# Kernel tuning notes

Hardware: AMD Instinct MI355X
Metric: run time of the kernel (lower is better)

## Reference

```python
import jax, jax.numpy as jnp
import numpy as np

D = 1024      # model dim
NSEQ = 4      # packed sequences
SEQ = 8192    # tokens per sequence
L = NSEQ * SEQ
EPS = 1e-4    # prob clamp in dechunk


def setup_inputs() -> dict:
    key = jax.random.key(0)
    ks = jax.random.split(key, 7)
    s = 1.0 / np.sqrt(D)
    mk = lambda k: jax.random.normal(k, (D, D), jnp.float32) * s
    return {
        'x': jax.random.normal(ks[0], (1, L, D), jnp.float32),
        'Wq': mk(ks[1]), 'Wk': mk(ks[2]), 'Wr': mk(ks[3]),
        'We': mk(ks[4]), 'Wm': mk(ks[5]), 'Wd': mk(ks[6]),
        'cu_seqlens': jnp.arange(NSEQ + 1, dtype=jnp.int32) * SEQ,
    }


def _normalize(v):
    n = jnp.linalg.norm(v, axis=-1, keepdims=True)
    return v / jnp.maximum(n, 1e-12)


def _forward(x, Wq, Wk, Wr, We, Wm, Wd, cu_seqlens):
    # encoder (pointwise linear)
    enc = jnp.einsum('bld,ed->ble', x, We)                  # [1,L,D]
    residual = jnp.einsum('bld,ed->ble', enc, Wr)           # residual_proj

    # Router: cosine similarity of adjacent tokens
    q = _normalize(jnp.einsum('bld,ed->ble', enc[:, :-1], Wq))
    k = _normalize(jnp.einsum('bld,ed->ble', enc[:, 1:], Wk))
    p = 0.5 * (1.0 - jnp.sum(q * k, axis=-1))               # [1,L-1]
    p = jnp.pad(p, ((0, 0), (1, 0)), constant_values=1.0)[0]  # [L]
    p = p.at[cu_seqlens[:-1]].set(1.0)                      # force boundary at seq starts
    mask = p > 0.5                                          # boundary_mask
    sel = jnp.where(mask, p, 1.0 - p)                       # selected_prob

    # main network on compressed tokens (pointwise -> compute in full layout,
    # non-boundary positions are never read by the scan below)
    m = jnp.einsum('bld,ed->ble', enc, Wm)[0]               # [L,D]

    # dechunk == mamba scan with A=-1, N=1: EMA h_t=(1-p)h + p*u at boundaries,
    # held (a=1) elsewhere; plug_back gather == held state. Reset at seq starts.
    pc = jnp.clip(p, EPS, 1.0 - EPS)
    starts = jnp.zeros(L, bool).at[cu_seqlens[:-1]].set(True)
    a = jnp.where(starts, 0.0, jnp.where(mask, 1.0 - pc, 1.0))[:, None]  # [L,1]
    b = jnp.where(mask[:, None], pc[:, None] * m, 0.0)                    # [L,D]

    def comb(c1, c2):
        a1, b1 = c1
        a2, b2 = c2
        return (a1 * a2, a2 * b1 + b2)

    _, y = jax.lax.associative_scan(comb, (a, b), axis=0)   # y: [L,D] dechunked

    # straight-through: forward multiplies by 1, backward passes grad to sel
    st = sel + jax.lax.stop_gradient(1.0 - sel)
    out = y[None] * st[None, :, None] + residual
    out = jnp.einsum('bld,ed->ble', out, Wd)                # decoder
    return out


def reference(x, Wq, Wk, Wr, We, Wm, Wd, cu_seqlens):
    return _forward(x, Wq, Wk, Wr, We, Wm, Wd, cu_seqlens)
```

## Files before the change

kernel.cpp:

```cpp
#include <hip/hip_runtime.h>
#include <math.h>

#define D_DIM 1024
#define CL 512

typedef __attribute__((ext_vector_type(8))) short short8;
typedef __attribute__((ext_vector_type(4))) float f32x4;
typedef unsigned short u16;

__device__ __forceinline__ u16 f2bf(float f) {
    unsigned int u = __float_as_uint(f);
    u += 0x7fff + ((u >> 16) & 1);
    return (u16)(u >> 16);
}
__device__ __forceinline__ float bf2f(u16 h) {
    return __uint_as_float((unsigned int)h << 16);
}

#define GLOAD16(g, l) __builtin_amdgcn_global_load_lds(                      \
        (const __attribute__((address_space(1))) void*)(g),                  \
        (__attribute__((address_space(3))) void*)(l), 16, 0, 0)
#define SBAR()   __builtin_amdgcn_s_barrier()
#define SCHED0() __builtin_amdgcn_sched_barrier(0)
#define PRIO(x)  __builtin_amdgcn_s_setprio(x)
#define WAITVM(N) asm volatile("s_waitcnt vmcnt(" #N ")" ::: "memory")


template<int EPI, int NPAIR>
__global__ __launch_bounds__(512) void gemm256(const u16* __restrict__ A1,
                                               const u16* __restrict__ W1,
                                               const u16* __restrict__ A2,
                                               const u16* __restrict__ W2,
                                               float* __restrict__ Cf,
                                               u16* __restrict__ Cb) {
    constexpr int NT = NPAIR * 32;
    __shared__ u16 lds[4 * 16384];
    __shared__ float nsum[4][256];
    const int tid = threadIdx.x;
    const int lane = tid & 63, wid = tid >> 6;
    const int wm = wid >> 2, wn = wid & 3;
    const int fr = lane & 15, fq = lane >> 4;
    const int row0 = blockIdx.x * 256, col0 = blockIdx.y * 256;
    const int r0s = tid >> 2, c0s = tid & 3;

    int offA[8], offB[4];
#pragma unroll
    for (int i = 0; i < 8; ++i) {
        const int r = wm * 128 + i * 16 + fr;
        offA[i] = r * 64 + ((fq ^ ((r >> 1) & 3)) << 4);
    }
#pragma unroll
    for (int j = 0; j < 4; ++j) {
        const int r = wn * 64 + j * 16 + fr;
        offB[j] = r * 64 + ((fq ^ ((r >> 1) & 3)) << 4);
    }

    auto stageA = [&](int s) {
        const u16* src = (NPAIR == 2 && s >= 32) ? A2 : A1;
        const int k0 = (NPAIR == 2 ? (s & 31) : s) * 32;
        char* dst = (char*)lds + (s & 3) * 32768;
#pragma unroll
        for (int j = 0; j < 2; ++j) {
            const int r = j * 128 + r0s;
            const int c = c0s ^ ((r >> 1) & 3);
            GLOAD16(src + (size_t)(row0 + r) * D_DIM + k0 + c * 8,
                    dst + j * 8192 + tid * 16);
        }
    };
    auto stageB = [&](int s) {
        const u16* src = (NPAIR == 2 && s >= 32) ? W2 : W1;
        const int k0 = (NPAIR == 2 ? (s & 31) : s) * 32;
        char* dst = (char*)lds + (s & 3) * 32768 + 16384;
#pragma unroll
        for (int j = 0; j < 2; ++j) {
            const int r = j * 128 + r0s;
            const int c = c0s ^ ((r >> 1) & 3);
            GLOAD16(src + (size_t)(col0 + r) * D_DIM + k0 + c * 8,
                    dst + j * 8192 + tid * 16);
        }
    };

    f32x4 acc[8][4];
#pragma unroll
    for (int i = 0; i < 8; ++i)
#pragma unroll
        for (int j = 0; j < 4; ++j) acc[i][j] = (f32x4){0.f, 0.f, 0.f, 0.f};

    stageA(0); stageB(0); stageA(1); stageB(1); stageA(2); stageB(2);
    WAITVM(8); SBAR(); SCHED0();

    for (int t = 0; t < NT; ++t) {
        const char* buf  = (const char*)lds + (t & 3) * 32768;
        const char* bufB = buf + 16384;
        short8 af[8], bf[4];
#pragma unroll
        for (int i = 0; i < 4; ++i) af[i] = *(const short8*)(buf + offA[i]);
#pragma unroll
        for (int j = 0; j < 4; ++j) bf[j] = *(const short8*)(bufB + offB[j]);
        if (t + 3 < NT) stageA(t + 3);
        SBAR();
        PRIO(1);
#pragma unroll
        for (int i = 0; i < 4; ++i)
#pragma unroll
            for (int j = 0; j < 4; ++j)
                acc[i][j] = __builtin_amdgcn_mfma_f32_16x16x32_bf16(af[i], bf[j], acc[i][j], 0, 0, 0);
        PRIO(0);
#pragma unroll
        for (int i = 4; i < 8; ++i) af[i] = *(const short8*)(buf + offA[i]);
        if (t + 3 < NT) stageB(t + 3);
        SBAR();
        PRIO(1);
#pragma unroll
        for (int i = 4; i < 8; ++i)
#pragma unroll
            for (int j = 0; j < 4; ++j)
                acc[i][j] = __builtin_amdgcn_mfma_f32_16x16x32_bf16(af[i], bf[j], acc[i][j], 0, 0, 0);
        PRIO(0);
        if (t + 1 < NT) {
            if (t + 3 < NT)      { WAITVM(8); }
            else if (t + 2 < NT) { WAITVM(4); }
            else                 { WAITVM(0); }
            SBAR(); SCHED0();
        }
    }

    if (EPI == 2) {
#pragma unroll
        for (int i = 0; i < 8; ++i)
#pragma unroll
            for (int rr = 0; rr < 4; ++rr) {
                float s = acc[i][0][rr] * acc[i][0][rr] + acc[i][1][rr] * acc[i][1][rr]
                        + acc[i][2][rr] * acc[i][2][rr] + acc[i][3][rr] * acc[i][3][rr];
#pragma unroll
                for (int off = 1; off < 16; off <<= 1) s += __shfl_xor(s, off);
                if (fr == 0) nsum[wn][wm * 128 + i * 16 + fq * 4 + rr] = s;
            }
        __syncthreads();
        if (tid < 256)
            Cf[(size_t)blockIdx.y * (gridDim.x * 256) + row0 + tid] =
                nsum[0][tid] + nsum[1][tid] + nsum[2][tid] + nsum[3][tid];
    } else {
#pragma unroll
        for (int i = 0; i < 8; ++i)
#pragma unroll
            for (int j = 0; j < 4; ++j) {
                const int r0 = row0 + wm * 128 + i * 16 + fq * 4;
                const int c  = col0 + wn * 64 + j * 16 + fr;
#pragma unroll
                for (int rr = 0; rr < 4; ++rr) {
                    if (EPI == 0) Cb[(size_t)(r0 + rr) * D_DIM + c] = f2bf(acc[i][j][rr]);
                    else          Cf[(size_t)(r0 + rr) * D_DIM + c] = acc[i][j][rr];
                }
            }
    }
}

template<int EPI>
__global__ __launch_bounds__(512) void gemm_x3(const u16* __restrict__ Ah,
                                               const u16* __restrict__ Al,
                                               const u16* __restrict__ Wh,
                                               const u16* __restrict__ Wl,
                                               float* __restrict__ Cf,
                                               u16* __restrict__ Chi,
                                               u16* __restrict__ Clo) {
    constexpr int NT = 32;
    __shared__ u16 lds[3 * 24576];
    const int tid = threadIdx.x;
    const int lane = tid & 63, wid = tid >> 6;
    const int wm = wid >> 2, wn = wid & 3;
    const int fr = lane & 15, fq = lane >> 4;
    const int row0 = blockIdx.x * 128, col0 = blockIdx.y * 256;
    const int r0s = tid >> 2, c0s = tid & 3;

    int offA[4], offB[4];
#pragma unroll
    for (int i = 0; i < 4; ++i) {
        const int r = wm * 64 + i * 16 + fr;
        offA[i] = r * 64 + ((fq ^ ((r >> 1) & 3)) << 4);
    }
#pragma unroll
    for (int j = 0; j < 4; ++j) {
        const int r = wn * 64 + j * 16 + fr;
        offB[j] = r * 64 + ((fq ^ ((r >> 1) & 3)) << 4);
    }

    auto stageAhl = [&](int s) {
        char* base = (char*)lds + (s % 3) * 49152;
        const int r = r0s;
        const int c = c0s ^ ((r >> 1) & 3);
        const size_t g = (size_t)(row0 + r) * D_DIM + s * 32 + c * 8;
        GLOAD16(Ah + g, base + tid * 16);
        GLOAD16(Al + g, base + 8192 + tid * 16);
    };
    auto stageBh = [&](int s) {
        char* base = (char*)lds + (s % 3) * 49152 + 16384;
#pragma unroll
        for (int j = 0; j < 2; ++j) {
            const int r = j * 128 + r0s;
            const int c = c0s ^ ((r >> 1) & 3);
            GLOAD16(Wh + (size_t)(col0 + r) * D_DIM + s * 32 + c * 8,
                    base + j * 8192 + tid * 16);
        }
    };
    auto stageBl = [&](int s) {
        char* base = (char*)lds + (s % 3) * 49152 + 32768;
#pragma unroll
        for (int j = 0; j < 2; ++j) {
            const int r = j * 128 + r0s;
            const int c = c0s ^ ((r >> 1) & 3);
            GLOAD16(Wl + (size_t)(col0 + r) * D_DIM + s * 32 + c * 8,
                    base + j * 8192 + tid * 16);
        }
    };

    f32x4 acc[4][4];
#pragma unroll
    for (int i = 0; i < 4; ++i)
#pragma unroll
        for (int j = 0; j < 4; ++j) acc[i][j] = (f32x4){0.f, 0.f, 0.f, 0.f};

    stageAhl(0); stageBh(0); stageBl(0);
    stageAhl(1); stageBh(1); stageBl(1);
    WAITVM(6); SBAR(); SCHED0();

    for (int t = 0; t < NT; ++t) {
        const char* base = (const char*)lds + (t % 3) * 49152;
        short8 afh[4], afl[4], bfh[4], bfl[4];
#pragma unroll
        for (int i = 0; i < 4; ++i) afh[i] = *(const short8*)(base + offA[i]);
#pragma unroll
        for (int j = 0; j < 4; ++j) bfh[j] = *(const short8*)(base + 16384 + offB[j]);
        if (t + 2 < NT) stageBh(t + 2);
        SBAR();
        PRIO(1);
#pragma unroll
        for (int i = 0; i < 4; ++i)
#pragma unroll
            for (int j = 0; j < 4; ++j)
                acc[i][j] = __builtin_amdgcn_mfma_f32_16x16x32_bf16(afh[i], bfh[j], acc[i][j], 0, 0, 0);
        PRIO(0);
#pragma unroll
        for (int j = 0; j < 4; ++j) bfl[j] = *(const short8*)(base + 32768 + offB[j]);
        if (t + 2 < NT) stageBl(t + 2);
        SBAR();
        PRIO(1);
#pragma unroll
        for (int i = 0; i < 4; ++i)
#pragma unroll
            for (int j = 0; j < 4; ++j)
                acc[i][j] = __builtin_amdgcn_mfma_f32_16x16x32_bf16(afh[i], bfl[j], acc[i][j], 0, 0, 0);
        PRIO(0);
#pragma unroll
        for (int i = 0; i < 4; ++i) afl[i] = *(const short8*)(base + 8192 + offA[i]);
        if (t + 2 < NT) stageAhl(t + 2);
        SBAR();
        PRIO(1);
#pragma unroll
        for (int i = 0; i < 4; ++i)
#pragma unroll
            for (int j = 0; j < 4; ++j)
                acc[i][j] = __builtin_amdgcn_mfma_f32_16x16x32_bf16(afl[i], bfh[j], acc[i][j], 0, 0, 0);
        PRIO(0);
        if (t + 1 < NT) {
            if (t + 2 < NT) { WAITVM(6); }
            else            { WAITVM(0); }
            SBAR(); SCHED0();
        }
    }

#pragma unroll
    for (int i = 0; i < 4; ++i)
#pragma unroll
        for (int j = 0; j < 4; ++j) {
            const int r0 = row0 + wm * 64 + i * 16 + fq * 4;
            const int c  = col0 + wn * 64 + j * 16 + fr;
#pragma unroll
            for (int rr = 0; rr < 4; ++rr) {
                const float v = acc[i][j][rr];
                if (EPI == 0) {
                    const u16 h = f2bf(v);
                    Chi[(size_t)(r0 + rr) * D_DIM + c] = h;
                    Clo[(size_t)(r0 + rr) * D_DIM + c] = f2bf(v - bf2f(h));
                } else {
                    Cf[(size_t)(r0 + rr) * D_DIM + c] = v;
                }
            }
        }
}

__global__ __launch_bounds__(256) void gemm_bf16_nt(const u16* __restrict__ A,
                                                    const u16* __restrict__ W,
                                                    float* __restrict__ C,
                                                    u16* __restrict__ Cbf) {
    __shared__ u16 lA[128 * 32];
    __shared__ u16 lB[128 * 32];
    const int tid  = threadIdx.x;
    const int lane = tid & 63, wid = tid >> 6;
    const int wy = wid & 1, wx = wid >> 1;
    const int fr = lane & 15, fq = lane >> 4;
    const int row0 = blockIdx.x * 128;
    const int col0 = blockIdx.y * 128;

    const int rS   = tid >> 2;
    const int subS = (tid & 3) ^ ((rS >> 1) & 3);
    const u16* gA = A + (size_t)(row0 + rS) * D_DIM + subS * 8;
    const u16* gB = W + (size_t)(col0 + rS) * D_DIM + subS * 8;
    char* lA0 = (char*)lA + tid * 16;
    char* lB0 = (char*)lB + tid * 16;
    const size_t rowStep = (size_t)64 * D_DIM;

    int offA[4], offB[4];
#pragma unroll
    for (int i = 0; i < 4; ++i) {
        const int ra = wy * 64 + i * 16 + fr;
        const int rb = wx * 64 + i * 16 + fr;
        offA[i] = ra * 64 + ((fq ^ ((ra >> 1) & 3)) << 4);
        offB[i] = rb * 64 + ((fq ^ ((rb >> 1) & 3)) << 4);
    }

    f32x4 acc[4][4];
#pragma unroll
    for (int i = 0; i < 4; ++i)
#pragma unroll
        for (int j = 0; j < 4; ++j) acc[i][j] = (f32x4){0.f, 0.f, 0.f, 0.f};

    for (int k0 = 0; k0 < D_DIM; k0 += 32) {
        __syncthreads();
        GLOAD16(gA + k0, lA0);
        GLOAD16(gA + k0 + rowStep, lA0 + 4096);
        GLOAD16(gB + k0, lB0);
        GLOAD16(gB + k0 + rowStep, lB0 + 4096);
        __syncthreads();
        short8 af[4], bf[4];
#pragma unroll
        for (int i = 0; i < 4; ++i) af[i] = *(const short8*)((const char*)lA + offA[i]);
#pragma unroll
        for (int j = 0; j < 4; ++j) bf[j] = *(const short8*)((const char*)lB + offB[j]);
#pragma unroll
        for (int i = 0; i < 4; ++i)
#pragma unroll
            for (int j = 0; j < 4; ++j)
                acc[i][j] = __builtin_amdgcn_mfma_f32_16x16x32_bf16(af[i], bf[j], acc[i][j], 0, 0, 0);
    }
#pragma unroll
    for (int i = 0; i < 4; ++i)
#pragma unroll
        for (int j = 0; j < 4; ++j) {
            const int r0 = row0 + wy * 64 + i * 16 + fq * 4;
            const int c  = col0 + wx * 64 + j * 16 + fr;
            if (Cbf) {
#pragma unroll
                for (int r = 0; r < 4; ++r)
                    Cbf[(size_t)(r0 + r) * D_DIM + c] = f2bf(acc[i][j][r]);
            } else {
#pragma unroll
                for (int r = 0; r < 4; ++r)
                    C[(size_t)(r0 + r) * D_DIM + c] = acc[i][j][r];
            }
        }
}

__global__ void split_bf16(const float* __restrict__ src, u16* __restrict__ hi,
                           u16* __restrict__ lo, int n4) {
    int i = blockIdx.x * 256 + threadIdx.x;
    if (i >= n4) return;
    float4 v = ((const float4*)src)[i];
    ushort4 h, l;
    h.x = f2bf(v.x); l.x = f2bf(v.x - bf2f(h.x));
    h.y = f2bf(v.y); l.y = f2bf(v.y - bf2f(h.y));
    h.z = f2bf(v.z); l.z = f2bf(v.z - bf2f(h.z));
    h.w = f2bf(v.w); l.w = f2bf(v.w - bf2f(h.w));
    ((ushort4*)hi)[i] = h;
    ((ushort4*)lo)[i] = l;
}

__global__ void conv_bf16(const float* __restrict__ src, u16* __restrict__ dst, int n4) {
    int i = blockIdx.x * 256 + threadIdx.x;
    if (i >= n4) return;
    float4 v = ((const float4*)src)[i];
    ushort4 o = {f2bf(v.x), f2bf(v.y), f2bf(v.z), f2bf(v.w)};
    ((ushort4*)dst)[i] = o;
}

__global__ __launch_bounds__(256) void transpose_split(const float* __restrict__ W,
                                                       u16* __restrict__ Th,
                                                       u16* __restrict__ Tl) {
    __shared__ float tile[32][33];
    const int e0 = blockIdx.x * 32, d0 = blockIdx.y * 32;
    const int tx = threadIdx.x & 31, ty = threadIdx.x >> 5;
#pragma unroll
    for (int i = 0; i < 32; i += 8)
        tile[ty + i][tx] = W[(size_t)(e0 + ty + i) * D_DIM + d0 + tx];
    __syncthreads();
#pragma unroll
    for (int i = 0; i < 32; i += 8) {
        float v = tile[tx][ty + i];
        u16 h = f2bf(v);
        Th[(size_t)(d0 + ty + i) * D_DIM + e0 + tx] = h;
        if (Tl) Tl[(size_t)(d0 + ty + i) * D_DIM + e0 + tx] = f2bf(v - bf2f(h));
    }
}

__global__ void combine_norm(const float* __restrict__ partq, const float* __restrict__ partk,
                             float* __restrict__ nq, float* __restrict__ nk, int L) {
    int l = blockIdx.x * 256 + threadIdx.x;
    if (l >= L) return;
    float sq = 0.f, sk = 0.f;
#pragma unroll
    for (int j = 0; j < 4; ++j) {
        sq += partq[(size_t)j * L + l];
        sk += partk[(size_t)j * L + l];
    }
    nq[l] = sq; nk[l] = sk;
}

__global__ __launch_bounds__(256) void router_p2(const u16* __restrict__ ench,
                                                 const u16* __restrict__ encl,
                                                 const float* __restrict__ t,
                                                 const float* __restrict__ nq,
                                                 const float* __restrict__ nk,
                                                 float* __restrict__ p) {
    const int l = blockIdx.x + 1;
    ushort4 h  = ((const ushort4*)(ench + (size_t)(l - 1) * D_DIM))[threadIdx.x];
    ushort4 lo = ((const ushort4*)(encl + (size_t)(l - 1) * D_DIM))[threadIdx.x];
    float4  tv = ((const float4*)(t + (size_t)l * D_DIM))[threadIdx.x];
    float dot = (bf2f(h.x) + bf2f(lo.x)) * tv.x
              + (bf2f(h.y) + bf2f(lo.y)) * tv.y
              + (bf2f(h.z) + bf2f(lo.z)) * tv.z
              + (bf2f(h.w) + bf2f(lo.w)) * tv.w;
#pragma unroll
    for (int off = 32; off > 0; off >>= 1) dot += __shfl_down(dot, off);
    __shared__ float red[4];
    const int w = threadIdx.x >> 6;
    if ((threadIdx.x & 63) == 0) red[w] = dot;
    __syncthreads();
    if (threadIdx.x == 0) {
        dot = red[0] + red[1] + red[2] + red[3];
        float dn = fmaxf(sqrtf(nq[l - 1]), 1e-12f) * fmaxf(sqrtf(nk[l]), 1e-12f);
        p[l] = 0.5f * (1.f - dot / dn);
    }
}

__global__ void finalize_pab(const float* __restrict__ p, const int* __restrict__ cu,
                             int nseq, float* __restrict__ a, float* __restrict__ bs,
                             int L) {
    int l = blockIdx.x * 256 + threadIdx.x;
    if (l >= L) return;
    bool start = false;
    for (int s = 0; s < nseq; ++s) start = start || (cu[s] == l);
    float pv = (l == 0) ? 1.f : p[l];
    if (start) pv = 1.f;
    bool mask = pv > 0.5f;
    float pc  = fminf(fmaxf(pv, 1e-4f), 1.f - 1e-4f);
    a[l]  = start ? 0.f : (mask ? (1.f - pc) : 1.f);
    bs[l] = mask ? pc : 0.f;
}

__global__ __launch_bounds__(256) void scan_local(const float* __restrict__ a,
                                                  const float* __restrict__ bs,
                                                  u16* __restrict__ m,
                                                  float* __restrict__ P) {
    __shared__ float a_s[CL], b_s[CL];
    const int chunk = blockIdx.x;
    const int d     = blockIdx.y * 256 + threadIdx.x;
    const int l0    = chunk * CL;
    for (int i = threadIdx.x; i < CL; i += 256) { a_s[i] = a[l0 + i]; b_s[i] = bs[l0 + i]; }
    __syncthreads();
    if (blockIdx.y == 0 && threadIdx.x == 0) {
        float pp = 1.f;
        for (int i = 0; i < CL; ++i) { pp *= a_s[i]; P[l0 + i] = pp; }
    }
    float h = 0.f;
    u16* mp = m + (size_t)l0 * D_DIM + d;
    for (int i = 0; i < CL; ++i) {
        float mv = bf2f(mp[(size_t)i * D_DIM]);
        h = fmaf(a_s[i], h, b_s[i] * mv);
        mp[(size_t)i * D_DIM] = f2bf(h);
    }
}

__global__ void scan_carry(const u16* __restrict__ y, const float* __restrict__ P,
                           float* __restrict__ carry, int nchunks) {
    const int d = blockIdx.x * 256 + threadIdx.x;
    float H = 0.f;
    for (int c = 0; c < nchunks; ++c) {
        carry[(size_t)c * D_DIM + d] = H;
        const float Ac = P[c * CL + (CL - 1)];
        const float Bc = bf2f(y[((size_t)c * CL + (CL - 1)) * D_DIM + d]);
        H = fmaf(Ac, H, Bc);
    }
}

__global__ void fixup_fuse(u16* __restrict__ y, const float* __restrict__ P,
                           const float* __restrict__ carry) {
    const size_t i8  = (size_t)blockIdx.x * 256 + threadIdx.x;
    const size_t idx = i8 * 8;
    const int l  = (int)(idx >> 10);
    const int dd = (int)(idx & 1023);
    const int c  = l >> 9;
    const float pl = P[l];
    short8 yv = *(short8*)(y + idx);
    const float4 c0 = *(const float4*)(carry + (size_t)c * D_DIM + dd);
    const float4 c1 = *(const float4*)(carry + (size_t)c * D_DIM + dd + 4);
    short8 o;
    o[0] = (short)f2bf(fmaf(pl, c0.x, bf2f((u16)yv[0])));
    o[1] = (short)f2bf(fmaf(pl, c0.y, bf2f((u16)yv[1])));
    o[2] = (short)f2bf(fmaf(pl, c0.z, bf2f((u16)yv[2])));
    o[3] = (short)f2bf(fmaf(pl, c0.w, bf2f((u16)yv[3])));
    o[4] = (short)f2bf(fmaf(pl, c1.x, bf2f((u16)yv[4])));
    o[5] = (short)f2bf(fmaf(pl, c1.y, bf2f((u16)yv[5])));
    o[6] = (short)f2bf(fmaf(pl, c1.z, bf2f((u16)yv[6])));
    o[7] = (short)f2bf(fmaf(pl, c1.w, bf2f((u16)yv[7])));
    *(short8*)(y + idx) = o;
}

extern "C" void kernel_launch(void* const* d_in, const int* in_sizes, int n_in,
                              void* d_out, int out_size, void* d_ws, size_t ws_size,
                              hipStream_t stream) {
    const float* x  = (const float*)d_in[0];
    const float* Wq = (const float*)d_in[1];
    const float* Wk = (const float*)d_in[2];
    const float* Wr = (const float*)d_in[3];
    const float* We = (const float*)d_in[4];
    const float* Wm = (const float*)d_in[5];
    const float* Wd = (const float*)d_in[6];
    const int*   cu = (const int*)d_in[7];
    const int L    = in_sizes[0] / D_DIM;
    const int nseq = in_sizes[7] - 1;

    const size_t LD2 = (size_t)L * D_DIM * 2;
    const size_t DD  = (size_t)D_DIM * D_DIM;
    const int nLD4 = L * D_DIM / 4;
    const int nDD4 = (int)(DD / 4);
    const int nchunks = L / CL;

    char* ws = (char*)d_ws;
    u16*   xh   = (u16*)ws;
    u16*   xl   = (u16*)(ws + LD2);
    float* tbuf = (float*)ws;
    u16*   mybuf= (u16*)ws;
    u16*   Wdb  = (u16*)(ws + LD2);
    u16*   Wdrb = Wdb + DD;
    u16*   ench = (u16*)(ws + 2 * LD2);
    u16*   encl = (u16*)(ws + 3 * LD2);
    float* p    = (float*)(ws + 4 * LD2);
    float* av   = p  + L;
    float* bs   = av + L;
    float* P    = bs + L;

    char* dob = (char*)d_out;
    u16* Weh   = (u16*)dob;
    u16* Wel   = (u16*)(dob + (2u << 20));
    u16* WqTh  = (u16*)(dob + (4u << 20));
    u16* WqTl  = (u16*)(dob + (6u << 20));
    u16* WkTh  = (u16*)(dob + (8u << 20));
    u16* WkTl  = (u16*)(dob + (10u << 20));
    float* Mf  = (float*)(dob + (12u << 20));
    u16* Mh    = (u16*)(dob + (16u << 20));
    u16* Ml    = (u16*)(dob + (18u << 20));
    u16* Wqb   = (u16*)(dob + (20u << 20));
    u16* Wkb   = (u16*)(dob + (22u << 20));
    u16* Wmb   = (u16*)(dob + (24u << 20));
    u16* WrTb  = (u16*)(dob + (26u << 20));
    float* partq = (float*)(dob + (28u << 20));
    float* partk = (float*)(dob + (29u << 20));
    float* nq    = (float*)(dob + (30u << 20));
    float* nk    = (float*)(dob + (30u << 20) + 131072);
    float* carry = (float*)(dob + (31u << 20));
    float* out = (float*)d_out;

    dim3 gX3L(L / 128, D_DIM / 256);
    dim3 gX3D(D_DIM / 128, D_DIM / 256);
    dim3 g256(L / 256, D_DIM / 256);
    dim3 gD(D_DIM / 128, D_DIM / 128);
    dim3 gT(D_DIM / 32, D_DIM / 32);

    split_bf16<<<(nLD4 + 255) / 256, 256, 0, stream>>>(x, xh, xl, nLD4);
    split_bf16<<<(nDD4 + 255) / 256, 256, 0, stream>>>(We, Weh, Wel, nDD4);
    gemm_x3<0><<<gX3L, 512, 0, stream>>>(xh, xl, Weh, Wel, nullptr, ench, encl);
    transpose_split<<<gT, 256, 0, stream>>>(Wq, WqTh, WqTl);
    transpose_split<<<gT, 256, 0, stream>>>(Wk, WkTh, WkTl);
    gemm_x3<1><<<gX3D, 512, 0, stream>>>(WqTh, WqTl, WkTh, WkTl, Mf, nullptr, nullptr);
    split_bf16<<<(nDD4 + 255) / 256, 256, 0, stream>>>(Mf, Mh, Ml, nDD4);
    gemm_x3<1><<<gX3L, 512, 0, stream>>>(ench, encl, Mh, Ml, tbuf, nullptr, nullptr);
    conv_bf16<<<(nDD4 + 255) / 256, 256, 0, stream>>>(Wq, Wqb, nDD4);
    conv_bf16<<<(nDD4 + 255) / 256, 256, 0, stream>>>(Wk, Wkb, nDD4);
    gemm256<2, 1><<<g256, 512, 0, stream>>>(ench, Wqb, nullptr, nullptr, partq, nullptr);
    gemm256<2, 1><<<g256, 512, 0, stream>>>(ench, Wkb, nullptr, nullptr, partk, nullptr);
    combine_norm<<<(L + 255) / 256, 256, 0, stream>>>(partq, partk, nq, nk, L);
    router_p2<<<L - 1, 256, 0, stream>>>(ench, encl, tbuf, nq, nk, p);
    finalize_pab<<<(L + 255) / 256, 256, 0, stream>>>(p, cu, nseq, av, bs, L);
    conv_bf16<<<(nDD4 + 255) / 256, 256, 0, stream>>>(Wm, Wmb, nDD4);
    gemm256<0, 1><<<g256, 512, 0, stream>>>(ench, Wmb, nullptr, nullptr, nullptr, mybuf);
    dim3 gsl(nchunks, D_DIM / 256);
    scan_local<<<gsl, 256, 0, stream>>>(av, bs, mybuf, P);
    scan_carry<<<D_DIM / 256, 256, 0, stream>>>(mybuf, P, carry, nchunks);
    fixup_fuse<<<(size_t)L * D_DIM / 8 / 256, 256, 0, stream>>>(mybuf, P, carry);
    transpose_split<<<gT, 256, 0, stream>>>(Wr, WrTb, nullptr);
    conv_bf16<<<(nDD4 + 255) / 256, 256, 0, stream>>>(Wd, Wdb, nDD4);
    gemm_bf16_nt<<<gD, 256, 0, stream>>>(Wdb, WrTb, nullptr, Wdrb);
    gemm256<1, 2><<<g256, 512, 0, stream>>>(mybuf, Wdb, ench, Wdrb, out, nullptr);
}
```

Measured before the change: 1.008 ms.

## Fold decoder into scan operands and fuse router dot/norm into GEMM epilogues

Because the scan is linear per channel, it can run on enc·(Wd·Wm)^T instead of enc·Wm^T. The residual path is precomputed as enc·(Wd·Wr)^T, so the final decoder GEMM is replaced by an elementwise fixup that writes fp32 output directly. The router dot product is fused into the x3 GEMM epilogue, removing the fp32 t buffer and the per-row router kernel. A new dual-output norm2 GEMM computes the q and k norms in one pass, and the combine, router and finalize kernels are merged. The cost is an extra DxD weight product and rounding the scan input to bf16 after the decoder fold, which may change accuracy.

```diff
diff --git a/kernel.cpp b/kernel.cpp
--- a/kernel.cpp
+++ b/kernel.cpp
@@ -26,16 +26,13 @@
 #define WAITVM(N) asm volatile("s_waitcnt vmcnt(" #N ")" ::: "memory")
 
 
-template<int EPI, int NPAIR>
+template<int EPI>
 __global__ __launch_bounds__(512) void gemm256(const u16* __restrict__ A1,
                                                const u16* __restrict__ W1,
-                                               const u16* __restrict__ A2,
-                                               const u16* __restrict__ W2,
                                                float* __restrict__ Cf,
                                                u16* __restrict__ Cb) {
-    constexpr int NT = NPAIR * 32;
+    constexpr int NT = 32;
     __shared__ u16 lds[4 * 16384];
-    __shared__ float nsum[4][256];
     const int tid = threadIdx.x;
     const int lane = tid & 63, wid = tid >> 6;
     const int wm = wid >> 2, wn = wid & 3;
@@ -56,26 +53,24 @@
     }
 
     auto stageA = [&](int s) {
-        const u16* src = (NPAIR == 2 && s >= 32) ? A2 : A1;
-        const int k0 = (NPAIR == 2 ? (s & 31) : s) * 32;
+        const int k0 = s * 32;
         char* dst = (char*)lds + (s & 3) * 32768;
 #pragma unroll
         for (int j = 0; j < 2; ++j) {
             const int r = j * 128 + r0s;
             const int c = c0s ^ ((r >> 1) & 3);
-            GLOAD16(src + (size_t)(row0 + r) * D_DIM + k0 + c * 8,
+            GLOAD16(A1 + (size_t)(row0 + r) * D_DIM + k0 + c * 8,
                     dst + j * 8192 + tid * 16);
         }
     };
     auto stageB = [&](int s) {
-        const u16* src = (NPAIR == 2 && s >= 32) ? W2 : W1;
-        const int k0 = (NPAIR == 2 ? (s & 31) : s) * 32;
+        const int k0 = s * 32;
         char* dst = (char*)lds + (s & 3) * 32768 + 16384;
 #pragma unroll
         for (int j = 0; j < 2; ++j) {
             const int r = j * 128 + r0s;
             const int c = c0s ^ ((r >> 1) & 3);
-            GLOAD16(src + (size_t)(col0 + r) * D_DIM + k0 + c * 8,
+            GLOAD16(W1 + (size_t)(col0 + r) * D_DIM + k0 + c * 8,
                     dst + j * 8192 + tid * 16);
         }
     };
@@ -125,35 +120,18 @@
         }
     }
 
-    if (EPI == 2) {
-#pragma unroll
-        for (int i = 0; i < 8; ++i)
+#pragma unroll
+    for (int i = 0; i < 8; ++i)
+#pragma unroll
+        for (int j = 0; j < 4; ++j) {
+            const int r0 = row0 + wm * 128 + i * 16 + fq * 4;
+            const int c  = col0 + wn * 64 + j * 16 + fr;
 #pragma unroll
             for (int rr = 0; rr < 4; ++rr) {
-                float s = acc[i][0][rr] * acc[i][0][rr] + acc[i][1][rr] * acc[i][1][rr]
-                        + acc[i][2][rr] * acc[i][2][rr] + acc[i][3][rr] * acc[i][3][rr];
-#pragma unroll
-                for (int off = 1; off < 16; off <<= 1) s += __shfl_xor(s, off);
-                if (fr == 0) nsum[wn][wm * 128 + i * 16 + fq * 4 + rr] = s;
+                if (EPI == 0) Cb[(size_t)(r0 + rr) * D_DIM + c] = f2bf(acc[i][j][rr]);
+                else          Cf[(size_t)(r0 + rr) * D_DIM + c] = acc[i][j][rr];
             }
-        __syncthreads();
-        if (tid < 256)
-            Cf[(size_t)blockIdx.y * (gridDim.x * 256) + row0 + tid] =
-                nsum[0][tid] + nsum[1][tid] + nsum[2][tid] + nsum[3][tid];
-    } else {
-#pragma unroll
-        for (int i = 0; i < 8; ++i)
-#pragma unroll
-            for (int j = 0; j < 4; ++j) {
-                const int r0 = row0 + wm * 128 + i * 16 + fq * 4;
-                const int c  = col0 + wn * 64 + j * 16 + fr;
-#pragma unroll
-                for (int rr = 0; rr < 4; ++rr) {
-                    if (EPI == 0) Cb[(size_t)(r0 + rr) * D_DIM + c] = f2bf(acc[i][j][rr]);
-                    else          Cf[(size_t)(r0 + rr) * D_DIM + c] = acc[i][j][rr];
-                }
-            }
-    }
+        }
 }
 
 template<int EPI>
@@ -163,7 +141,10 @@
                                                const u16* __restrict__ Wl,
                                                float* __restrict__ Cf,
                                                u16* __restrict__ Chi,
-                                               u16* __restrict__ Clo) {
+                                               u16* __restrict__ Clo,
+                                               const u16* __restrict__ Eh,
+                                               const u16* __restrict__ El,
+                                               float* __restrict__ Pd) {
     constexpr int NT = 32;
     __shared__ u16 lds[3 * 24576];
     const int tid = threadIdx.x;
@@ -269,6 +250,31 @@
         }
     }
 
+    if (EPI == 2) {
+        const int Ltot = gridDim.x * 128;
+#pragma unroll
+        for (int i = 0; i < 4; ++i)
+#pragma unroll
+            for (int rr = 0; rr < 4; ++rr) {
+                const int r = row0 + wm * 64 + i * 16 + fq * 4 + rr;
+                float s = 0.f;
+#pragma unroll
+                for (int j = 0; j < 4; ++j) {
+                    const int c = col0 + wn * 64 + j * 16 + fr;
+                    float e = 0.f;
+                    if (r > 0) {
+                        const size_t o = (size_t)(r - 1) * D_DIM + c;
+                        e = bf2f(Eh[o]) + bf2f(El[o]);
+                    }
+                    s += acc[i][j][rr] * e;
+                }
+#pragma unroll
+                for (int off = 1; off < 16; off <<= 1) s += __shfl_xor(s, off);
+                if (fr == 0)
+                    Pd[(size_t)(blockIdx.y * 4 + wn) * Ltot + r] = s;
+            }
+        return;
+    }
 #pragma unroll
     for (int i = 0; i < 4; ++i)
 #pragma unroll
@@ -285,6 +291,130 @@
                 } else {
                     Cf[(size_t)(r0 + rr) * D_DIM + c] = v;
                 }
+            }
+        }
+}
+
+__global__ __launch_bounds__(512) void norm2(const u16* __restrict__ A,
+                                             const u16* __restrict__ Bq,
+                                             const u16* __restrict__ Bk,
+                                             float* __restrict__ Pq,
+                                             float* __restrict__ Pk) {
+    constexpr int NT = 32;
+    __shared__ u16 lds[3 * 20480];
+    const int tid = threadIdx.x;
+    const int lane = tid & 63, wid = tid >> 6;
+    const int wm = wid >> 2, wn = wid & 3;
+    const int fr = lane & 15, fq = lane >> 4;
+    const int row0 = blockIdx.x * 128, col0 = blockIdx.y * 256;
+    const int r0s = tid >> 2, c0s = tid & 3;
+
+    int offA[4], offB[4];
+#pragma unroll
+    for (int i = 0; i < 4; ++i) {
+        const int r = wm * 64 + i * 16 + fr;
+        offA[i] = r * 64 + ((fq ^ ((r >> 1) & 3)) << 4);
+    }
+#pragma unroll
+    for (int j = 0; j < 4; ++j) {
+        const int r = wn * 64 + j * 16 + fr;
+        offB[j] = r * 64 + ((fq ^ ((r >> 1) & 3)) << 4);
+    }
+
+    auto stageA = [&](int s) {
+        char* base = (char*)lds + (s % 3) * 40960;
+        const int r = r0s;
+        const int c = c0s ^ ((r >> 1) & 3);
+        GLOAD16(A + (size_t)(row0 + r) * D_DIM + s * 32 + c * 8, base + tid * 16);
+    };
+    auto stageBq = [&](int s) {
+        char* base = (char*)lds + (s % 3) * 40960 + 8192;
+#pragma unroll
+        for (int j = 0; j < 2; ++j) {
+            const int r = j * 128 + r0s;
+            const int c = c0s ^ ((r >> 1) & 3);
+            GLOAD16(Bq + (size_t)(col0 + r) * D_DIM + s * 32 + c * 8,
+                    base + j * 8192 + tid * 16);
+        }
+    };
+    auto stageBk = [&](int s) {
+        char* base = (char*)lds + (s % 3) * 40960 + 24576;
+#pragma unroll
+        for (int j = 0; j < 2; ++j) {
+            const int r = j * 128 + r0s;
+            const int c = c0s ^ ((r >> 1) & 3);
+            GLOAD16(Bk + (size_t)(col0 + r) * D_DIM + s * 32 + c * 8,
+                    base + j * 8192 + tid * 16);
+        }
+    };
+
+    f32x4 accq[4][4], acck[4][4];
+#pragma unroll
+    for (int i = 0; i < 4; ++i)
+#pragma unroll
+        for (int j = 0; j < 4; ++j) {
+            accq[i][j] = (f32x4){0.f, 0.f, 0.f, 0.f};
+            acck[i][j] = (f32x4){0.f, 0.f, 0.f, 0.f};
+        }
+
+    stageA(0); stageBq(0); stageBk(0);
+    stageA(1); stageBq(1); stageBk(1);
+    WAITVM(5); SBAR(); SCHED0();
+
+    for (int t = 0; t < NT; ++t) {
+        const char* base = (const char*)lds + (t % 3) * 40960;
+        short8 af[4], bq[4], bk[4];
+#pragma unroll
+        for (int i = 0; i < 4; ++i) af[i] = *(const short8*)(base + offA[i]);
+#pragma unroll
+        for (int j = 0; j < 4; ++j) bq[j] = *(const short8*)(base + 8192 + offB[j]);
+        if (t + 2 < NT) { stageA(t + 2); stageBq(t + 2); }
+        SBAR();
+        PRIO(1);
+#pragma unroll
+        for (int i = 0; i < 4; ++i)
+#pragma unroll
+            for (int j = 0; j < 4; ++j)
+                accq[i][j] = __builtin_amdgcn_mfma_f32_16x16x32_bf16(af[i], bq[j], accq[i][j], 0, 0, 0);
+        PRIO(0);
+#pragma unroll
+        for (int j = 0; j < 4; ++j) bk[j] = *(const short8*)(base + 24576 + offB[j]);
+        if (t + 2 < NT) stageBk(t + 2);
+        SBAR();
+        PRIO(1);
+#pragma unroll
+        for (int i = 0; i < 4; ++i)
+#pragma unroll
+            for (int j = 0; j < 4; ++j)
+                acck[i][j] = __builtin_amdgcn_mfma_f32_16x16x32_bf16(af[i], bk[j], acck[i][j], 0, 0, 0);
+        PRIO(0);
+        if (t + 1 < NT) {
+            if (t + 2 < NT) { WAITVM(5); }
+            else            { WAITVM(0); }
+            SBAR(); SCHED0();
+        }
+    }
+
+    const int Ltot = gridDim.x * 128;
+#pragma unroll
+    for (int i = 0; i < 4; ++i)
+#pragma unroll
+        for (int rr = 0; rr < 4; ++rr) {
+            const int r = row0 + wm * 64 + i * 16 + fq * 4 + rr;
+            float sq = 0.f, sk = 0.f;
+#pragma unroll
+            for (int j = 0; j < 4; ++j) {
+                sq += accq[i][j][rr] * accq[i][j][rr];
+                sk += acck[i][j][rr] * acck[i][j][rr];
+            }
+#pragma unroll
+            for (int off = 1; off < 16; off <<= 1) {
+                sq += __shfl_xor(sq, off);
+                sk += __shfl_xor(sk, off);
+            }
+            if (fr == 0) {
+                Pq[(size_t)(blockIdx.y * 4 + wn) * Ltot + r] = sq;
+                Pk[(size_t)(blockIdx.y * 4 + wn) * Ltot + r] = sk;
             }
         }
 }
@@ -402,54 +532,29 @@
     }
 }
 
-__global__ void combine_norm(const float* __restrict__ partq, const float* __restrict__ partk,
-                             float* __restrict__ nq, float* __restrict__ nk, int L) {
+__global__ void combine_router(const float* __restrict__ pd,
+                               const float* __restrict__ pq,
+                               const float* __restrict__ pk,
+                               const int* __restrict__ cu, int nseq,
+                               float* __restrict__ a, float* __restrict__ bs,
+                               int L) {
     int l = blockIdx.x * 256 + threadIdx.x;
     if (l >= L) return;
-    float sq = 0.f, sk = 0.f;
-#pragma unroll
-    for (int j = 0; j < 4; ++j) {
-        sq += partq[(size_t)j * L + l];
-        sk += partk[(size_t)j * L + l];
-    }
-    nq[l] = sq; nk[l] = sk;
-}
-
-__global__ __launch_bounds__(256) void router_p2(const u16* __restrict__ ench,
-                                                 const u16* __restrict__ encl,
-                                                 const float* __restrict__ t,
-                                                 const float* __restrict__ nq,
-                                                 const float* __restrict__ nk,
-                                                 float* __restrict__ p) {
-    const int l = blockIdx.x + 1;
-    ushort4 h  = ((const ushort4*)(ench + (size_t)(l - 1) * D_DIM))[threadIdx.x];
-    ushort4 lo = ((const ushort4*)(encl + (size_t)(l - 1) * D_DIM))[threadIdx.x];
-    float4  tv = ((const float4*)(t + (size_t)l * D_DIM))[threadIdx.x];
-    float dot = (bf2f(h.x) + bf2f(lo.x)) * tv.x
-              + (bf2f(h.y) + bf2f(lo.y)) * tv.y
-              + (bf2f(h.z) + bf2f(lo.z)) * tv.z
-              + (bf2f(h.w) + bf2f(lo.w)) * tv.w;
-#pragma unroll
-    for (int off = 32; off > 0; off >>= 1) dot += __shfl_down(dot, off);
-    __shared__ float red[4];
-    const int w = threadIdx.x >> 6;
-    if ((threadIdx.x & 63) == 0) red[w] = dot;
-    __syncthreads();
-    if (threadIdx.x == 0) {
-        dot = red[0] + red[1] + red[2] + red[3];
-        float dn = fmaxf(sqrtf(nq[l - 1]), 1e-12f) * fmaxf(sqrtf(nk[l]), 1e-12f);
-        p[l] = 0.5f * (1.f - dot / dn);
-    }
-}
-
-__global__ void finalize_pab(const float* __restrict__ p, const int* __restrict__ cu,
-                             int nseq, float* __restrict__ a, float* __restrict__ bs,
-                             int L) {
-    int l = blockIdx.x * 256 + threadIdx.x;
-    if (l >= L) return;
+    float dot = 0.f, q2 = 0.f, k2 = 0.f;
+#pragma unroll
+    for (int j = 0; j < 16; ++j) {
+        dot += pd[(size_t)j * L + l];
+        k2  += pk[(size_t)j * L + l];
+        if (l > 0) q2 += pq[(size_t)j * L + l - 1];
+    }
+    float pv;
+    if (l == 0) pv = 1.f;
+    else {
+        float dn = fmaxf(sqrtf(q2), 1e-12f) * fmaxf(sqrtf(k2), 1e-12f);
+        pv = 0.5f * (1.f - dot / dn);
+    }
     bool start = false;
     for (int s = 0; s < nseq; ++s) start = start || (cu[s] == l);
-    float pv = (l == 0) ? 1.f : p[l];
     if (start) pv = 1.f;
     bool mask = pv > 0.5f;
     float pc  = fminf(fmaxf(pv, 1e-4f), 1.f - 1e-4f);
@@ -492,27 +597,30 @@
     }
 }
 
-__global__ void fixup_fuse(u16* __restrict__ y, const float* __restrict__ P,
-                           const float* __restrict__ carry) {
+__global__ void fixup_out(const u16* __restrict__ z, const float* __restrict__ P,
+                          const float* __restrict__ carry, const u16* __restrict__ r,
+                          float* __restrict__ out) {
     const size_t i8  = (size_t)blockIdx.x * 256 + threadIdx.x;
     const size_t idx = i8 * 8;
     const int l  = (int)(idx >> 10);
     const int dd = (int)(idx & 1023);
     const int c  = l >> 9;
     const float pl = P[l];
-    short8 yv = *(short8*)(y + idx);
+    short8 zv = *(const short8*)(z + idx);
+    short8 rv = *(const short8*)(r + idx);
     const float4 c0 = *(const float4*)(carry + (size_t)c * D_DIM + dd);
     const float4 c1 = *(const float4*)(carry + (size_t)c * D_DIM + dd + 4);
-    short8 o;
-    o[0] = (short)f2bf(fmaf(pl, c0.x, bf2f((u16)yv[0])));
-    o[1] = (short)f2bf(fmaf(pl, c0.y, bf2f((u16)yv[1])));
-    o[2] = (short)f2bf(fmaf(pl, c0.z, bf2f((u16)yv[2])));
-    o[3] = (short)f2bf(fmaf(pl, c0.w, bf2f((u16)yv[3])));
-    o[4] = (short)f2bf(fmaf(pl, c1.x, bf2f((u16)yv[4])));
-    o[5] = (short)f2bf(fmaf(pl, c1.y, bf2f((u16)yv[5])));
-    o[6] = (short)f2bf(fmaf(pl, c1.z, bf2f((u16)yv[6])));
-    o[7] = (short)f2bf(fmaf(pl, c1.w, bf2f((u16)yv[7])));
-    *(short8*)(y + idx) = o;
+    float4 o0, o1;
+    o0.x = fmaf(pl, c0.x, bf2f((u16)zv[0])) + bf2f((u16)rv[0]);
+    o0.y = fmaf(pl, c0.y, bf2f((u16)zv[1])) + bf2f((u16)rv[1]);
+    o0.z = fmaf(pl, c0.z, bf2f((u16)zv[2])) + bf2f((u16)rv[2]);
+    o0.w = fmaf(pl, c0.w, bf2f((u16)zv[3])) + bf2f((u16)rv[3]);
+    o1.x = fmaf(pl, c1.x, bf2f((u16)zv[4])) + bf2f((u16)rv[4]);
+    o1.y = fmaf(pl, c1.y, bf2f((u16)zv[5])) + bf2f((u16)rv[5]);
+    o1.z = fmaf(pl, c1.z, bf2f((u16)zv[6])) + bf2f((u16)rv[6]);
+    o1.w = fmaf(pl, c1.w, bf2f((u16)zv[7])) + bf2f((u16)rv[7]);
+    *(float4*)(out + idx)     = o0;
+    *(float4*)(out + idx + 4) = o1;
 }
 
 extern "C" void kernel_launch(void* const* d_in, const int* in_sizes, int n_in,
@@ -538,16 +646,14 @@
     char* ws = (char*)d_ws;
     u16*   xh   = (u16*)ws;
     u16*   xl   = (u16*)(ws + LD2);
-    float* tbuf = (float*)ws;
-    u16*   mybuf= (u16*)ws;
-    u16*   Wdb  = (u16*)(ws + LD2);
-    u16*   Wdrb = Wdb + DD;
+    u16*   zbuf = (u16*)ws;
+    u16*   rbuf = (u16*)(ws + LD2);
     u16*   ench = (u16*)(ws + 2 * LD2);
     u16*   encl = (u16*)(ws + 3 * LD2);
-    float* p    = (float*)(ws + 4 * LD2);
-    float* av   = p  + L;
+    float* av   = (float*)(ws + 4 * LD2);
     float* bs   = av + L;
     float* P    = bs + L;
+    float* carry= P  + L;
 
     char* dob = (char*)d_out;
     u16* Weh   = (u16*)dob;
@@ -561,13 +667,14 @@
     u16* Ml    = (u16*)(dob + (18u << 20));
     u16* Wqb   = (u16*)(dob + (20u << 20));
     u16* Wkb   = (u16*)(dob + (22u << 20));
-    u16* Wmb   = (u16*)(dob + (24u << 20));
+    u16* WmTb  = (u16*)(dob + (24u << 20));
     u16* WrTb  = (u16*)(dob + (26u << 20));
-    float* partq = (float*)(dob + (28u << 20));
-    float* partk = (float*)(dob + (29u << 20));
-    float* nq    = (float*)(dob + (30u << 20));
-    float* nk    = (float*)(dob + (30u << 20) + 131072);
-    float* carry = (float*)(dob + (31u << 20));
+    u16* Wdb   = (u16*)(dob + (28u << 20));
+    u16* Wdmb  = (u16*)(dob + (30u << 20));
+    u16* Wdrb  = (u16*)(dob + (32u << 20));
+    float* partdot = (float*)(dob + (34u << 20));
+    float* partnq  = (float*)(dob + (36u << 20));
+    float* partnk  = (float*)(dob + (38u << 20));
     float* out = (float*)d_out;
 
     dim3 gX3L(L / 128, D_DIM / 256);
@@ -578,27 +685,29 @@
 
     split_bf16<<<(nLD4 + 255) / 256, 256, 0, stream>>>(x, xh, xl, nLD4);
     split_bf16<<<(nDD4 + 255) / 256, 256, 0, stream>>>(We, Weh, Wel, nDD4);
-    gemm_x3<0><<<gX3L, 512, 0, stream>>>(xh, xl, Weh, Wel, nullptr, ench, encl);
+    gemm_x3<0><<<gX3L, 512, 0, stream>>>(xh, xl, Weh, Wel, nullptr, ench, encl,
+                                         nullptr, nullptr, nullptr);
     transpose_split<<<gT, 256, 0, stream>>>(Wq, WqTh, WqTl);
     transpose_split<<<gT, 256, 0, stream>>>(Wk, WkTh, WkTl);
-    gemm_x3<1><<<gX3D, 512, 0, stream>>>(WqTh, WqTl, WkTh, WkTl, Mf, nullptr, nullptr);
+    gemm_x3<1><<<gX3D, 512, 0, stream>>>(WqTh, WqTl, WkTh, WkTl, Mf, nullptr, nullptr,
+                                         nullptr, nullptr, nullptr);
     split_bf16<<<(nDD4 + 255) / 256, 256, 0, stream>>>(Mf, Mh, Ml, nDD4);
-    gemm_x3<1><<<gX3L, 512, 0, stream>>>(ench, encl, Mh, Ml, tbuf, nullptr, nullptr);
+    gemm_x3<2><<<gX3L, 512, 0, stream>>>(ench, encl, Mh, Ml, nullptr, nullptr, nullptr,
+                                         ench, encl, partdot);
     conv_bf16<<<(nDD4 + 255) / 256, 256, 0, stream>>>(Wq, Wqb, nDD4);
     conv_bf16<<<(nDD4 + 255) / 256, 256, 0, stream>>>(Wk, Wkb, nDD4);
-    gemm256<2, 1><<<g256, 512, 0, stream>>>(ench, Wqb, nullptr, nullptr, partq, nullptr);
-    gemm256<2, 1><<<g256, 512, 0, stream>>>(ench, Wkb, nullptr, nullptr, partk, nullptr);
-    combine_norm<<<(L + 255) / 256, 256, 0, stream>>>(partq, partk, nq, nk, L);
-    router_p2<<<L - 1, 256, 0, stream>>>(ench, encl, tbuf, nq, nk, p);
-    finalize_pab<<<(L + 255) / 256, 256, 0, stream>>>(p, cu, nseq, av, bs, L);
-    conv_bf16<<<(nDD4 + 255) / 256, 256, 0, stream>>>(Wm, Wmb, nDD4);
-    gemm256<0, 1><<<g256, 512, 0, stream>>>(ench, Wmb, nullptr, nullptr, nullptr, mybuf);
+    norm2<<<gX3L, 512, 0, stream>>>(ench, Wqb, Wkb, partnq, partnk);
+    combine_router<<<(L + 255) / 256, 256, 0, stream>>>(partdot, partnq, partnk,
+                                                        cu, nseq, av, bs, L);
+    conv_bf16<<<(nDD4 + 255) / 256, 256, 0, stream>>>(Wd, Wdb, nDD4);
+    transpose_split<<<gT, 256, 0, stream>>>(Wm, WmTb, nullptr);
+    transpose_split<<<gT, 256, 0, stream>>>(Wr, WrTb, nullptr);
+    gemm_bf16_nt<<<gD, 256, 0, stream>>>(Wdb, WmTb, nullptr, Wdmb);
+    gemm_bf16_nt<<<gD, 256, 0, stream>>>(Wdb, WrTb, nullptr, Wdrb);
+    gemm256<0><<<g256, 512, 0, stream>>>(ench, Wdmb, nullptr, zbuf);
+    gemm256<0><<<g256, 512, 0, stream>>>(ench, Wdrb, nullptr, rbuf);
     dim3 gsl(nchunks, D_DIM / 256);
-    scan_local<<<gsl, 256, 0, stream>>>(av, bs, mybuf, P);
-    scan_carry<<<D_DIM / 256, 256, 0, stream>>>(mybuf, P, carry, nchunks);
-    fixup_fuse<<<(size_t)L * D_DIM / 8 / 256, 256, 0, stream>>>(mybuf, P, carry);
-    transpose_split<<<gT, 256, 0, stream>>>(Wr, WrTb, nullptr);
-    conv_bf16<<<(nDD4 + 255) / 256, 256, 0, stream>>>(Wd, Wdb, nDD4);
-    gemm_bf16_nt<<<gD, 256, 0, stream>>>(Wdb, WrTb, nullptr, Wdrb);
-    gemm256<1, 2><<<g256, 512, 0, stream>>>(mybuf, Wdb, ench, Wdrb, out, nullptr);
-}
+    scan_local<<<gsl, 256, 0, stream>>>(av, bs, zbuf, P);
+    scan_carry<<<D_DIM / 256, 256, 0, stream>>>(zbuf, P, carry, nchunks);
+    fixup_out<<<(size_t)L * D_DIM / 8 / 256, 256, 0, stream>>>(zbuf, P, carry, rbuf, out);
+}
```

New measurement: 1.002 ms. About the same (-0.6%).
